# Performance work log

Measured on AMD Instinct MI355X. Metric: run time of the kernel, lower is better.

Reference implementation:

```python
import jax, jax.numpy as jnp
import numpy as np

BETA = 0.25
COMMIT_W = 1.0
EPS = 1e-6
N_E, E_DIM, C = 8192, 256, 256
B, H, W = 16, 32, 32


def setup_inputs() -> dict:
    key = jax.random.key(0)
    k1, k2, k3 = jax.random.split(key, 3)
    z = jax.random.normal(k1, (B, C, H, W), jnp.float32)
    frozen_codebook = jax.random.normal(k2, (N_E, E_DIM), jnp.float32) * (E_DIM ** -0.5)
    w_transform = jax.random.normal(k3, (C, E_DIM), jnp.float32) * (E_DIM ** -0.5)
    return {"z": z, "frozen_codebook": frozen_codebook, "w_transform": w_transform}


def _rotate_to(src, tgt):
    # Rotation trick: Householder-style rotation of src onto direction of tgt.
    sg = jax.lax.stop_gradient
    norm_src = jnp.linalg.norm(src, axis=-1, keepdims=True)
    norm_tgt = jnp.linalg.norm(tgt, axis=-1, keepdims=True)
    u = src / jnp.clip(norm_src, EPS)          # normalized source
    q = tgt / jnp.clip(norm_tgt, EPS)          # normalized target
    w = u + q
    w = sg(w / jnp.clip(jnp.linalg.norm(w, axis=-1, keepdims=True), EPS))
    u = sg(u)
    q = sg(q)
    e = src  # gradients flow through e only (rotation matrix is detached)
    rotated = (e
               - 2.0 * jnp.sum(e * w, axis=-1, keepdims=True) * w
               + 2.0 * jnp.sum(e * u, axis=-1, keepdims=True) * q)
    return rotated * sg(norm_tgt / jnp.clip(norm_src, EPS))


def reference(z, frozen_codebook, w_transform):
    z = z.astype(jnp.float32)
    zc = jnp.transpose(z, (0, 2, 3, 1))          # b h w c
    z_flat = zc.reshape(-1, zc.shape[-1])        # [N, C]
    codebook = frozen_codebook @ w_transform.T   # [n_e, C] (Linear, no bias)

    # squared L2 distances, argmin under no_grad
    d = (jnp.sum(z_flat ** 2, axis=1, keepdims=True)
         + jnp.sum(codebook ** 2, axis=1)
         - 2.0 * jnp.einsum('bd,nd->bn', z_flat, codebook))
    indices = jnp.argmin(jax.lax.stop_gradient(d), axis=1)  # [N]

    z_q_flat = codebook[indices]                 # [N, C]
    sg = jax.lax.stop_gradient
    loss = (jnp.mean((sg(z_flat) - z_q_flat) ** 2)
            + BETA * jnp.mean((z_flat - sg(z_q_flat)) ** 2)) * COMMIT_W

    z_q_flat = _rotate_to(z_flat, z_q_flat)      # rotation trick
    z_q = z_q_flat.reshape(zc.shape)             # b h w c
    z_q = jnp.transpose(z_q, (0, 3, 1, 2))       # b c h w
    return z_q, loss, indices
```

## Files before the change

kernel.cpp:

```cpp
#include <hip/hip_runtime.h>
#include <math.h>

typedef unsigned short u16;
typedef unsigned int   u32;

#define B_   16
#define C_   256
#define HW_  1024
#define N_   16384
#define NE_  8192
#define K_   256
#define NSPLIT 4
#define CPS  2048
#define NZQ  4194304

typedef _Float16 f16x8 __attribute__((ext_vector_type(8)));
typedef float    f32x16 __attribute__((ext_vector_type(16)));


__device__ __forceinline__ u16 f2h(float x) {
    union { _Float16 h; u16 u; } c;
    c.h = (_Float16)x;
    return c.u;
}

__global__ __launch_bounds__(256) void k_pre(
        const float* __restrict__ z, const float* __restrict__ f,
        const float* __restrict__ w, float* __restrict__ zf,
        u16* __restrict__ zh, float* __restrict__ cb, u16* __restrict__ cbh,
        double* __restrict__ c2part) {
    __shared__ float tileT[32][33];
    __shared__ float Fs[16][68];
    __shared__ float Ws[16][68];
    int bid = blockIdx.x;
    int tid = threadIdx.x;

    if (bid >= 512) {
        int b2  = bid - 512;
        int hw0 = (b2 & 31) * 32;
        int c0  = ((b2 >> 5) & 7) * 32;
        int b   = b2 >> 8;
        int tx = tid & 31;
        int ty = tid >> 5;
        #pragma unroll
        for (int i = 0; i < 4; ++i) {
            int c = c0 + ty + i * 8;
            tileT[ty + i * 8][tx] = z[((size_t)b * C_ + c) * HW_ + hw0 + tx];
        }
        __syncthreads();
        #pragma unroll
        for (int i = 0; i < 4; ++i) {
            int hw = hw0 + ty + i * 8;
            size_t o = ((size_t)b * HW_ + hw) * C_ + c0 + tx;
            float v = tileT[tx][ty + i * 8];
            zf[o] = v;
            zh[o] = f2h(v);
        }
        return;
    }

    int n0 = (bid & 127) * 64;
    int c0 = (bid >> 7) * 64;
    int tx = tid & 15, ty = tid >> 4;
    int nl = tid >> 2;
    int kq = (tid & 3) * 4;
    float acc[4][4] = {};
    float4 fv = *(const float4*)&f[(size_t)(n0 + nl) * K_ + kq];
    float4 wv = *(const float4*)&w[(size_t)(c0 + nl) * K_ + kq];
    for (int kb = 0; kb < K_; kb += 16) {
        __syncthreads();
        Fs[kq + 0][nl] = fv.x; Fs[kq + 1][nl] = fv.y; Fs[kq + 2][nl] = fv.z; Fs[kq + 3][nl] = fv.w;
        Ws[kq + 0][nl] = wv.x; Ws[kq + 1][nl] = wv.y; Ws[kq + 2][nl] = wv.z; Ws[kq + 3][nl] = wv.w;
        __syncthreads();
        if (kb + 16 < K_) {
            fv = *(const float4*)&f[(size_t)(n0 + nl) * K_ + kb + 16 + kq];
            wv = *(const float4*)&w[(size_t)(c0 + nl) * K_ + kb + 16 + kq];
        }
        #pragma unroll
        for (int k = 0; k < 16; ++k) {
            float4 a = *(float4*)&Fs[k][ty * 4];
            float4 b = *(float4*)&Ws[k][tx * 4];
            float av[4] = {a.x, a.y, a.z, a.w};
            float bv[4] = {b.x, b.y, b.z, b.w};
            #pragma unroll
            for (int i = 0; i < 4; ++i)
                #pragma unroll
                for (int j = 0; j < 4; ++j)
                    acc[i][j] += av[i] * bv[j];
        }
    }
    #pragma unroll
    for (int i = 0; i < 4; ++i) {
        size_t o = (size_t)(n0 + ty * 4 + i) * K_ + c0 + tx * 4;
        *(float4*)&cb[o] = make_float4(acc[i][0], acc[i][1], acc[i][2], acc[i][3]);
        *(ushort4*)&cbh[o] = make_ushort4(f2h(acc[i][0]), f2h(acc[i][1]),
                                          f2h(acc[i][2]), f2h(acc[i][3]));
        double ps = (double)acc[i][0] * acc[i][0] + (double)acc[i][1] * acc[i][1]
                  + (double)acc[i][2] * acc[i][2] + (double)acc[i][3] * acc[i][3];
        #pragma unroll
        for (int off = 8; off; off >>= 1) ps += __shfl_down(ps, off, 16);
        if (tx == 0) c2part[(size_t)(n0 + ty * 4 + i) * 4 + (c0 >> 6)] = ps;
    }
}

__device__ __forceinline__ void ld_lds16(const void* g, void* l) {
    __builtin_amdgcn_global_load_lds((const __attribute__((address_space(1))) void*)g,
                                     (__attribute__((address_space(3))) void*)l, 16, 0, 0);
}

#define INS(M1, M2, U) { u32 t_ = min(M1, U); u32 h_ = max(M1, U); M1 = t_; M2 = min(M2, h_); }

#define SCORE16(ACC, M1, M2, CGBASE, C2B) do {                                    \
    u32 ib_ = (u32)(code0 + (CGBASE));                                            \
    _Pragma("unroll")                                                             \
    for (int h = 0; h < 4; ++h) {                                                 \
        float4 cv = *(const float4*)&(C2B)[(CGBASE) + 8 * h];                     \
        u32 u0 = (((u32)fmaf(-8192.f, (ACC)[4*h+0], cv.x)) << 13) + ib_ + 8*h + 0; \
        u32 u1 = (((u32)fmaf(-8192.f, (ACC)[4*h+1], cv.y)) << 13) + ib_ + 8*h + 1; \
        u32 u2 = (((u32)fmaf(-8192.f, (ACC)[4*h+2], cv.z)) << 13) + ib_ + 8*h + 2; \
        u32 u3 = (((u32)fmaf(-8192.f, (ACC)[4*h+3], cv.w)) << 13) + ib_ + 8*h + 3; \
        INS(M1, M2, u0); INS(M1, M2, u1); INS(M1, M2, u2); INS(M1, M2, u3);       \
    }                                                                             \
} while (0)

#define WAITVM(N) { asm volatile("s_waitcnt vmcnt(" #N ")" ::: "memory"); \
                    __builtin_amdgcn_s_barrier();                          \
                    __builtin_amdgcn_sched_barrier(0); }

__global__ __launch_bounds__(256, 2) void k_scan_mfma(
        const u16* __restrict__ zh, const u16* __restrict__ cbh,
        const double* __restrict__ c2part, double* __restrict__ c2d,
        int* __restrict__ t2i) {
    __shared__ __align__(16) u16 sA[4][8192];
    __shared__ __align__(16) float c2s[2048];

    int r0    = blockIdx.x * 128;
    int split = blockIdx.y;
    int tid  = threadIdx.x;
    int wave = tid >> 6, lane = tid & 63;
    int l31 = lane & 31, q = lane >> 5;
    int ra = ((wave & 1) << 6) + l31;

    const u16* zp = zh + (size_t)(r0 + ((wave >> 1) << 6) + l31) * K_ + q * 8;
    f16x8 zr0[16], zr1[16];
    #pragma unroll
    for (int t = 0; t < 16; ++t) {
        zr0[t] = *(const f16x8*)&zp[t * 16];
        zr1[t] = *(const f16x8*)&zp[32 * K_ + t * 16];
    }

    size_t ga[4]; u32 la[4];
    #pragma unroll
    for (int it = 0; it < 4; ++it) {
        int S = (it * 4 + wave) * 64 + lane;
        int row = S >> 3, u = S & 7;
        ga[it] = (size_t)row * K_ + (u ^ (row & 7)) * 8;
        la[it] = (u32)(it * 4 + wave) * 512;
    }

    u32 m1a = 0xFFFFFFFFu, m2a = 0xFFFFFFFFu;
    u32 m1b = 0xFFFFFFFFu, m2b = 0xFFFFFFFFu;

    const u16* cb0 = cbh + (size_t)split * CPS * K_;

    auto STAGE = [&](int s) {
        const u16* Ab = cb0 + (size_t)(s >> 2) * (128 * K_) + (s & 3) * 64;
        u16* d = &sA[s & 3][0];
        #pragma unroll
        for (int it = 0; it < 4; ++it) ld_lds16(Ab + ga[it], d + la[it]);
    };

    f32x16 acc0 = (f32x16){}, acc1 = (f32x16){}, acc2 = (f32x16){}, acc3 = (f32x16){};

    auto COMPUTE = [&](int ct, int kb) {
        const u16* sAb = &sA[kb][0];
        __builtin_amdgcn_s_setprio(1);
        #pragma unroll
        for (int ks = 0; ks < 4; ++ks) {
            u32 u8 = (u32)(((ks * 2 + q) ^ (l31 & 7)) * 8);
            f16x8 af0 = *(const f16x8*)&sAb[(u32)ra * 64 + u8];
            f16x8 af1 = *(const f16x8*)&sAb[(u32)ra * 64 + 2048 + u8];
            acc0 = __builtin_amdgcn_mfma_f32_32x32x16_f16(af0, zr0[kb * 4 + ks], acc0, 0, 0, 0);
            acc1 = __builtin_amdgcn_mfma_f32_32x32x16_f16(af1, zr0[kb * 4 + ks], acc1, 0, 0, 0);
            acc2 = __builtin_amdgcn_mfma_f32_32x32x16_f16(af0, zr1[kb * 4 + ks], acc2, 0, 0, 0);
            acc3 = __builtin_amdgcn_mfma_f32_32x32x16_f16(af1, zr1[kb * 4 + ks], acc3, 0, 0, 0);
        }
        __builtin_amdgcn_s_setprio(0);
        if (kb == 3) {
            int code0 = split * CPS + ct * 128;
            const float* C2B = &c2s[ct * 128];
            int cga = ((wave & 1) << 6) + (q << 2);
            int cgb = cga + 32;
            SCORE16(acc0, m1a, m2a, cga, C2B);
            SCORE16(acc1, m1a, m2a, cgb, C2B);
            SCORE16(acc2, m1b, m2b, cga, C2B);
            SCORE16(acc3, m1b, m2b, cgb, C2B);
            acc0 = (f32x16){}; acc1 = (f32x16){}; acc2 = (f32x16){}; acc3 = (f32x16){};
        }
    };

    {
        const double* cp = c2part + (size_t)split * CPS * 4;
        #pragma unroll
        for (int r = 0; r < 8; ++r) {
            int row = tid * 8 + r;
            const double* pr = cp + (size_t)row * 4;
            double s = (pr[0] + pr[1]) + (pr[2] + pr[3]);
            c2s[row] = (float)(s * 4096.0 + 262144.0);
            if (blockIdx.x == 0) c2d[split * CPS + row] = s;
        }
    }
    STAGE(0); STAGE(1);
    __syncthreads();
    __builtin_amdgcn_sched_barrier(0);

    for (int ct = 0; ct < 15; ++ct) {
        #pragma unroll
        for (int kb = 0; kb < 4; ++kb) {
            STAGE(ct * 4 + kb + 2);
            WAITVM(8);
            COMPUTE(ct, kb);
        }
    }
    STAGE(62); WAITVM(8); COMPUTE(15, 0);
    STAGE(63); WAITVM(8); COMPUTE(15, 1);
    WAITVM(4);            COMPUTE(15, 2);
    WAITVM(0);            COMPUTE(15, 3);

    {
        u32 o1 = __shfl_xor(m1a, 32, 64), o2 = __shfl_xor(m2a, 32, 64);
        u32 h = max(m1a, o1); m1a = min(m1a, o1); m2a = min(min(m2a, o2), h);
        o1 = __shfl_xor(m1b, 32, 64); o2 = __shfl_xor(m2b, 32, 64);
        h = max(m1b, o1); m1b = min(m1b, o1); m2b = min(min(m2b, o2), h);
    }
    u32* mbuf = (u32*)&sA[0][0];
    if (q == 0) {
        int base = ((wave * 2 + 0) * 32 + l31) * 2;
        mbuf[base] = m1a; mbuf[base + 1] = m2a;
        base = ((wave * 2 + 1) * 32 + l31) * 2;
        mbuf[base] = m1b; mbuf[base + 1] = m2b;
    }
    __syncthreads();
    if (tid < 128) {
        int zr = tid, wp = zr >> 6, zg = (zr >> 5) & 1, l = zr & 31;
        int iA = (((wp * 2 + 0) * 2 + zg) * 32 + l) * 2;
        int iB = (((wp * 2 + 1) * 2 + zg) * 32 + l) * 2;
        u32 a1 = mbuf[iA], a2 = mbuf[iA + 1];
        u32 b1 = mbuf[iB], b2 = mbuf[iB + 1];
        u32 h  = max(a1, b1), f1 = min(a1, b1);
        u32 f2 = min(min(a2, b2), h);
        size_t o = ((size_t)split * N_ + (r0 + zr)) * 2;
        t2i[o] = (int)f1;
        t2i[o + 1] = (int)f2;
    }
}

__global__ __launch_bounds__(256) void k_finalize(
        const float* __restrict__ zf, const float* __restrict__ cb,
        const double* __restrict__ c2d, const u32* __restrict__ t2i,
        float* __restrict__ out) {
    __shared__ int   bidx[16];
    __shared__ float wsum[4];
    __shared__ float tile[16][260];
    int n0 = blockIdx.x * 16;
    int tid = threadIdx.x;
    int wv = tid >> 6, lane = tid & 63;
    int h = lane >> 5, l5 = lane & 31;
    const u32 W = 160u << 13;

    for (int rr = 0; rr < 4; ++rr) {
        int n = n0 + wv * 4 + rr;
        u32 pk[4];
        u32 b1 = 0xFFFFFFFFu, b2 = 0xFFFFFFFFu;
        #pragma unroll
        for (int p = 0; p < 4; ++p) {
            u32 pa = t2i[((size_t)p * N_ + n) * 2 + 0];
            u32 pb = t2i[((size_t)p * N_ + n) * 2 + 1];
            pk[p] = h ? pb : pa;
            INS(b1, b2, pa); INS(b1, b2, pb);
        }

        int bi;
        if (b2 - b1 >= W) {
            bi = (int)(b1 & 0x1FFFu);
        } else {
            const float* zp = zf + (size_t)n * K_;
            float4 za = *(const float4*)&zp[l5 * 4];
            float4 zb = *(const float4*)&zp[l5 * 4 + 128];
            int cid[4];
            #pragma unroll
            for (int p = 0; p < 4; ++p) cid[p] = (int)(pk[p] & 0x1FFFu);
            double c2p[4];
            #pragma unroll
            for (int p = 0; p < 4; ++p) c2p[p] = c2d[cid[p]];
            float4 cva = *(const float4*)&cb[(size_t)cid[0] * K_ + l5 * 4];
            float4 cvb = *(const float4*)&cb[(size_t)cid[0] * K_ + l5 * 4 + 128];

            double bs = 1e300; bi = 0x7fffffff;
            #pragma unroll
            for (int p = 0; p < 4; ++p) {
                float4 ca = cva, cbv = cvb;
                if (p < 3) {
                    cva = *(const float4*)&cb[(size_t)cid[p + 1] * K_ + l5 * 4];
                    cvb = *(const float4*)&cb[(size_t)cid[p + 1] * K_ + l5 * 4 + 128];
                }
                double acc = (double)za.x * ca.x + (double)za.y * ca.y
                           + (double)za.z * ca.z + (double)za.w * ca.w
                           + (double)zb.x * cbv.x + (double)zb.y * cbv.y
                           + (double)zb.z * cbv.z + (double)zb.w * cbv.w;
                #pragma unroll
                for (int off = 1; off < 32; off <<= 1) acc += __shfl_xor(acc, off, 32);
                double sc = c2p[p] - 2.0 * acc;
                int    ci = cid[p];
                double so = __shfl_xor(sc, 32, 64);
                int    io = __shfl_xor(ci, 32, 64);
                double s0 = h ? so : sc;  int i0 = h ? io : ci;
                double s1 = h ? sc : so;  int i1 = h ? ci : io;
                if (s0 < bs || (s0 == bs && i0 < bi)) { bs = s0; bi = i0; }
                if (s1 < bs || (s1 == bs && i1 < bi)) { bs = s1; bi = i1; }
            }
        }
        if (lane == 0) {
            bidx[wv * 4 + rr] = bi;
            out[(size_t)NZQ + 1 + n] = (float)bi;
        }
    }
    __syncthreads();

    float accl = 0.f;
    for (int l = 0; l < 16; ++l) {
        int n = n0 + l;
        int bi = bidx[l];
        float zq = cb[(size_t)bi * K_ + tid];
        float d  = zf[(size_t)n * K_ + tid] - zq;
        accl += d * d;
        tile[l][tid] = zq;
    }
    #pragma unroll
    for (int off = 32; off; off >>= 1) accl += __shfl_down(accl, off, 64);
    if ((tid & 63) == 0) wsum[tid >> 6] = accl;
    __syncthreads();
    if (tid == 0)
        atomicAdd(out + NZQ, (wsum[0] + wsum[1] + wsum[2] + wsum[3]) * (1.25f / (float)NZQ));
    int b = n0 >> 10, hw0 = n0 & 1023;
    #pragma unroll
    for (int g = 0; g < 4; ++g) {
        float4 v = make_float4(tile[g * 4 + 0][tid], tile[g * 4 + 1][tid],
                               tile[g * 4 + 2][tid], tile[g * 4 + 3][tid]);
        *(float4*)&out[((size_t)b * C_ + tid) * HW_ + hw0 + g * 4] = v;
    }
}

extern "C" void kernel_launch(void* const* d_in, const int* in_sizes, int n_in,
                              void* d_out, int out_size, void* d_ws, size_t ws_size,
                              hipStream_t stream) {
    const float* z  = (const float*)d_in[0];
    const float* fc = (const float*)d_in[1];
    const float* wt = (const float*)d_in[2];
    float* out = (float*)d_out;

    float* ws = (float*)d_ws;
    const size_t OFF_ZF   = 0;
    const size_t OFF_CB   = OFF_ZF + (size_t)N_ * K_;
    const size_t OFF_C2P  = OFF_CB + (size_t)NE_ * K_;
    const size_t OFF_C2D  = OFF_C2P + (size_t)NE_ * 8;
    const size_t OFF_T2I  = OFF_C2D + (size_t)NE_ * 2;
    const size_t OFF_ZH   = OFF_T2I + (size_t)NSPLIT * N_ * 2;
    const size_t OFF_CBH  = OFF_ZH + (size_t)N_ * K_ / 2;

    float*  zf     = ws + OFF_ZF;
    float*  cb     = ws + OFF_CB;
    double* c2part = (double*)(ws + OFF_C2P);
    double* c2d    = (double*)(ws + OFF_C2D);
    int*    t2i    = (int*)(ws + OFF_T2I);
    u16*    zh     = (u16*)(ws + OFF_ZH);
    u16*    cbh    = (u16*)(ws + OFF_CBH);

    k_pre<<<4608, 256, 0, stream>>>(z, fc, wt, zf, zh, cb, cbh, c2part);
    k_scan_mfma<<<dim3(N_ / 128, NSPLIT), 256, 0, stream>>>(zh, cbh, c2part, c2d, t2i);
    k_finalize<<<N_ / 16, 256, 0, stream>>>(zf, cb, c2d, (const u32*)t2i, out);
}
```

Baseline: 197.4 us.

## Compute codebook projection with split-fp16 MFMA instead of FP32 FMA

Replaces the scalar FP32 FMA tiled GEMM that forms the projected codebook with 32x32x16 fp16 MFMA instructions. Each fp32 operand is split into a high and a low fp16 part, and three MFMAs per tile recover near-fp32 accuracy. Tiles grow to 128x128 with 4 waves per block, so there are fewer GEMM blocks and the grid shrinks. The epilogue now writes scattered per-lane scalars and does 32-lane double shuffles for row norms. That adds store and shuffle cost, and the lo*lo term is dropped.

```diff
diff --git a/kernel.cpp b/kernel.cpp
--- a/kernel.cpp
+++ b/kernel.cpp
@@ -23,6 +23,11 @@
     c.h = (_Float16)x;
     return c.u;
 }
+__device__ __forceinline__ float h2f(u16 u) {
+    union { _Float16 h; u16 u; } c;
+    c.u = u;
+    return (float)c.h;
+}
 
 __global__ __launch_bounds__(256) void k_pre(
         const float* __restrict__ z, const float* __restrict__ f,
@@ -30,28 +35,28 @@
         u16* __restrict__ zh, float* __restrict__ cb, u16* __restrict__ cbh,
         double* __restrict__ c2part) {
     __shared__ float tileT[32][33];
-    __shared__ float Fs[16][68];
-    __shared__ float Ws[16][68];
+    __shared__ __align__(16) u16 sF[2][128][40];
+    __shared__ __align__(16) u16 sW[2][128][40];
     int bid = blockIdx.x;
     int tid = threadIdx.x;
 
-    if (bid >= 512) {
-        int b2  = bid - 512;
+    if (bid >= 128) {
+        int b2  = bid - 128;
         int hw0 = (b2 & 31) * 32;
-        int c0  = ((b2 >> 5) & 7) * 32;
+        int c0t = ((b2 >> 5) & 7) * 32;
         int b   = b2 >> 8;
         int tx = tid & 31;
         int ty = tid >> 5;
         #pragma unroll
         for (int i = 0; i < 4; ++i) {
-            int c = c0 + ty + i * 8;
+            int c = c0t + ty + i * 8;
             tileT[ty + i * 8][tx] = z[((size_t)b * C_ + c) * HW_ + hw0 + tx];
         }
         __syncthreads();
         #pragma unroll
         for (int i = 0; i < 4; ++i) {
             int hw = hw0 + ty + i * 8;
-            size_t o = ((size_t)b * HW_ + hw) * C_ + c0 + tx;
+            size_t o = ((size_t)b * HW_ + hw) * C_ + c0t + tx;
             float v = tileT[tx][ty + i * 8];
             zf[o] = v;
             zh[o] = f2h(v);
@@ -59,48 +64,108 @@
         return;
     }
 
-    int n0 = (bid & 127) * 64;
-    int c0 = (bid >> 7) * 64;
-    int tx = tid & 15, ty = tid >> 4;
-    int nl = tid >> 2;
-    int kq = (tid & 3) * 4;
-    float acc[4][4] = {};
-    float4 fv = *(const float4*)&f[(size_t)(n0 + nl) * K_ + kq];
-    float4 wv = *(const float4*)&w[(size_t)(c0 + nl) * K_ + kq];
-    for (int kb = 0; kb < K_; kb += 16) {
+    int n0 = (bid & 63) * 128;
+    int c0 = (bid >> 6) * 128;
+    int wave = tid >> 6, lane = tid & 63;
+    int l31 = lane & 31, q = lane >> 5;
+    int wn = wave & 1, wc = wave >> 1;
+    int rl = tid >> 1;
+    int dh = (tid & 1) * 16;
+
+    f32x16 acc00 = (f32x16){}, acc01 = (f32x16){}, acc10 = (f32x16){}, acc11 = (f32x16){};
+
+    float fr[16], wr[16];
+    {
+        const float* fp = &f[(size_t)(n0 + rl) * K_ + dh];
+        const float* wp = &w[(size_t)(c0 + rl) * K_ + dh];
+        #pragma unroll
+        for (int g = 0; g < 4; ++g) {
+            *(float4*)&fr[g * 4] = *(const float4*)&fp[g * 4];
+            *(float4*)&wr[g * 4] = *(const float4*)&wp[g * 4];
+        }
+    }
+
+    for (int s = 0; s < 8; ++s) {
         __syncthreads();
-        Fs[kq + 0][nl] = fv.x; Fs[kq + 1][nl] = fv.y; Fs[kq + 2][nl] = fv.z; Fs[kq + 3][nl] = fv.w;
-        Ws[kq + 0][nl] = wv.x; Ws[kq + 1][nl] = wv.y; Ws[kq + 2][nl] = wv.z; Ws[kq + 3][nl] = wv.w;
+        {
+            u16 fh[16], fl[16], wh[16], wl[16];
+            #pragma unroll
+            for (int j = 0; j < 16; ++j) {
+                u16 h = f2h(fr[j]); fh[j] = h; fl[j] = f2h(fr[j] - h2f(h));
+                h = f2h(wr[j]);     wh[j] = h; wl[j] = f2h(wr[j] - h2f(h));
+            }
+            #pragma unroll
+            for (int g = 0; g < 2; ++g) {
+                *(f16x8*)&sF[0][rl][dh + g * 8] = *(f16x8*)&fh[g * 8];
+                *(f16x8*)&sF[1][rl][dh + g * 8] = *(f16x8*)&fl[g * 8];
+                *(f16x8*)&sW[0][rl][dh + g * 8] = *(f16x8*)&wh[g * 8];
+                *(f16x8*)&sW[1][rl][dh + g * 8] = *(f16x8*)&wl[g * 8];
+            }
+        }
         __syncthreads();
-        if (kb + 16 < K_) {
-            fv = *(const float4*)&f[(size_t)(n0 + nl) * K_ + kb + 16 + kq];
-            wv = *(const float4*)&w[(size_t)(c0 + nl) * K_ + kb + 16 + kq];
-        }
-        #pragma unroll
-        for (int k = 0; k < 16; ++k) {
-            float4 a = *(float4*)&Fs[k][ty * 4];
-            float4 b = *(float4*)&Ws[k][tx * 4];
-            float av[4] = {a.x, a.y, a.z, a.w};
-            float bv[4] = {b.x, b.y, b.z, b.w};
-            #pragma unroll
-            for (int i = 0; i < 4; ++i)
-                #pragma unroll
-                for (int j = 0; j < 4; ++j)
-                    acc[i][j] += av[i] * bv[j];
-        }
-    }
-    #pragma unroll
-    for (int i = 0; i < 4; ++i) {
-        size_t o = (size_t)(n0 + ty * 4 + i) * K_ + c0 + tx * 4;
-        *(float4*)&cb[o] = make_float4(acc[i][0], acc[i][1], acc[i][2], acc[i][3]);
-        *(ushort4*)&cbh[o] = make_ushort4(f2h(acc[i][0]), f2h(acc[i][1]),
-                                          f2h(acc[i][2]), f2h(acc[i][3]));
-        double ps = (double)acc[i][0] * acc[i][0] + (double)acc[i][1] * acc[i][1]
-                  + (double)acc[i][2] * acc[i][2] + (double)acc[i][3] * acc[i][3];
-        #pragma unroll
-        for (int off = 8; off; off >>= 1) ps += __shfl_down(ps, off, 16);
-        if (tx == 0) c2part[(size_t)(n0 + ty * 4 + i) * 4 + (c0 >> 6)] = ps;
-    }
+        if (s < 7) {
+            const float* fp = &f[(size_t)(n0 + rl) * K_ + (s + 1) * 32 + dh];
+            const float* wp = &w[(size_t)(c0 + rl) * K_ + (s + 1) * 32 + dh];
+            #pragma unroll
+            for (int g = 0; g < 4; ++g) {
+                *(float4*)&fr[g * 4] = *(const float4*)&fp[g * 4];
+                *(float4*)&wr[g * 4] = *(const float4*)&wp[g * 4];
+            }
+        }
+        #pragma unroll
+        for (int ks = 0; ks < 2; ++ks) {
+            u32 uo = (u32)(ks * 2 + q) * 8;
+            int rA = wn * 64 + l31, rB = wc * 64 + l31;
+            f16x8 ah0 = *(const f16x8*)&sF[0][rA][uo];
+            f16x8 ah1 = *(const f16x8*)&sF[0][rA + 32][uo];
+            f16x8 al0 = *(const f16x8*)&sF[1][rA][uo];
+            f16x8 al1 = *(const f16x8*)&sF[1][rA + 32][uo];
+            f16x8 bh0 = *(const f16x8*)&sW[0][rB][uo];
+            f16x8 bh1 = *(const f16x8*)&sW[0][rB + 32][uo];
+            f16x8 bl0 = *(const f16x8*)&sW[1][rB][uo];
+            f16x8 bl1 = *(const f16x8*)&sW[1][rB + 32][uo];
+            acc00 = __builtin_amdgcn_mfma_f32_32x32x16_f16(al0, bh0, acc00, 0, 0, 0);
+            acc00 = __builtin_amdgcn_mfma_f32_32x32x16_f16(ah0, bl0, acc00, 0, 0, 0);
+            acc00 = __builtin_amdgcn_mfma_f32_32x32x16_f16(ah0, bh0, acc00, 0, 0, 0);
+            acc01 = __builtin_amdgcn_mfma_f32_32x32x16_f16(al0, bh1, acc01, 0, 0, 0);
+            acc01 = __builtin_amdgcn_mfma_f32_32x32x16_f16(ah0, bl1, acc01, 0, 0, 0);
+            acc01 = __builtin_amdgcn_mfma_f32_32x32x16_f16(ah0, bh1, acc01, 0, 0, 0);
+            acc10 = __builtin_amdgcn_mfma_f32_32x32x16_f16(al1, bh0, acc10, 0, 0, 0);
+            acc10 = __builtin_amdgcn_mfma_f32_32x32x16_f16(ah1, bl0, acc10, 0, 0, 0);
+            acc10 = __builtin_amdgcn_mfma_f32_32x32x16_f16(ah1, bh0, acc10, 0, 0, 0);
+            acc11 = __builtin_amdgcn_mfma_f32_32x32x16_f16(al1, bh1, acc11, 0, 0, 0);
+            acc11 = __builtin_amdgcn_mfma_f32_32x32x16_f16(ah1, bl1, acc11, 0, 0, 0);
+            acc11 = __builtin_amdgcn_mfma_f32_32x32x16_f16(ah1, bh1, acc11, 0, 0, 0);
+        }
+    }
+
+    #define EPI_A(AIDX, ACC0, ACC1) {                                             \
+        int rbase = n0 + wn * 64 + (AIDX) * 32 + 4 * q;                           \
+        double ps[16];                                                            \
+        _Pragma("unroll")                                                         \
+        for (int r = 0; r < 16; ++r) {                                            \
+            int nr = rbase + (r & 3) + 8 * (r >> 2);                              \
+            int col0 = c0 + wc * 64 + l31;                                        \
+            cb[(size_t)nr * K_ + col0] = (ACC0)[r];                               \
+            cbh[(size_t)nr * K_ + col0] = f2h((ACC0)[r]);                         \
+            cb[(size_t)nr * K_ + col0 + 32] = (ACC1)[r];                          \
+            cbh[(size_t)nr * K_ + col0 + 32] = f2h((ACC1)[r]);                    \
+            ps[r] = (double)(ACC0)[r] * (ACC0)[r] + (double)(ACC1)[r] * (ACC1)[r];\
+        }                                                                         \
+        _Pragma("unroll")                                                         \
+        for (int r = 0; r < 16; ++r) {                                            \
+            double v = ps[r];                                                     \
+            _Pragma("unroll")                                                     \
+            for (int off = 1; off < 32; off <<= 1) v += __shfl_xor(v, off, 32);   \
+            if (l31 == 0) {                                                       \
+                int nr = rbase + (r & 3) + 8 * (r >> 2);                          \
+                c2part[(size_t)nr * 4 + (c0 >> 6) + wc] = v;                      \
+            }                                                                     \
+        }                                                                         \
+    }
+    EPI_A(0, acc00, acc01);
+    EPI_A(1, acc10, acc11);
+    #undef EPI_A
 }
 
 __device__ __forceinline__ void ld_lds16(const void* g, void* l) {
@@ -376,7 +441,7 @@
     u16*    zh     = (u16*)(ws + OFF_ZH);
     u16*    cbh    = (u16*)(ws + OFF_CBH);
 
-    k_pre<<<4608, 256, 0, stream>>>(z, fc, wt, zf, zh, cb, cbh, c2part);
+    k_pre<<<4224, 256, 0, stream>>>(z, fc, wt, zf, zh, cb, cbh, c2part);
     k_scan_mfma<<<dim3(N_ / 128, NSPLIT), 256, 0, stream>>>(zh, cbh, c2part, c2d, t2i);
     k_finalize<<<N_ / 16, 256, 0, stream>>>(zf, cb, c2d, (const u32*)t2i, out);
 }
```

Measured after the change: 195.2 us. No clear change (-1.1%).
